# Kernel tuning notes

Hardware: AMD Instinct MI355X
Metric: run time of the kernel (lower is better)

The kernel has to match this reference:

```python
import jax, jax.numpy as jnp
import numpy as np

NUM_CELLS = 16384
NUM_CLASSES = 64
BATCH = 64


def setup_inputs() -> dict:
    key = jax.random.key(0)
    k1, k2 = jax.random.split(key)
    x = jax.random.normal(k1, (BATCH, NUM_CELLS, 1), dtype=jnp.float32)
    weights = jax.random.normal(k2, (NUM_CELLS, NUM_CLASSES, 3), dtype=jnp.float32)
    bias = jnp.zeros((NUM_CELLS, NUM_CLASSES), dtype=jnp.float32)
    return {"x": x, "weights": weights, "bias": bias}


def reference(x, weights, bias):
    # x: (B, N, 1); weights: (N, C, 3); bias: (N, C)
    xs = x[..., 0]                      # (B, N)
    left = jnp.roll(xs, 1, axis=1)      # x[:, i-1]
    right = jnp.roll(xs, -1, axis=1)    # x[:, i+1]
    # out[b,i,c] = left*W[i,c,0] + center*W[i,c,1] + right*W[i,c,2] + bias[i,c]
    out = (left[:, :, None] * weights[:, :, 0]
           + xs[:, :, None] * weights[:, :, 1]
           + right[:, :, None] * weights[:, :, 2]
           + bias)
    return 1.7159 * jnp.tanh(out * (2.0 / 3.0))
```

## Files before the change

kernel.cpp:

```cpp
#include <hip/hip_runtime.h>

#define N_CELLS   16384
#define N_CLASSES 64
#define BATCH     64
#define CPB       4

typedef float f32x4 __attribute__((ext_vector_type(4)));

__device__ __forceinline__ float agm_act(float s) {
    float az = fabsf(s);
    float e  = __expf(-1.3333333333f * az);
    float t  = __fdividef(1.0f - e, 1.0f + e);
    return copysignf(1.7159f * t, s);
}

__global__ __launch_bounds__(256) void mnl_kernel(
    const float* __restrict__ x,
    const float* __restrict__ w,
    const float* __restrict__ bias,
    float* __restrict__ out)
{
    const int t    = threadIdx.x;
    const int lane = t & 63;
    const int wid  = t >> 6;
    const int di   = lane >> 4;
    const int c4   = (lane & 15) * 4;
    const int i    = blockIdx.x * CPB + di;

    const int il = (i == 0)           ? N_CELLS - 1 : i - 1;
    const int ir = (i == N_CELLS - 1) ? 0           : i + 1;

    const float4* wv = reinterpret_cast<const float4*>(
        w + (size_t)i * (N_CLASSES * 3) + (size_t)c4 * 3);
    const float4 v0 = wv[0], v1 = wv[1], v2 = wv[2];
    const float wr[12] = { v0.x, v0.y, v0.z, v0.w,
                           v1.x, v1.y, v1.z, v1.w,
                           v2.x, v2.y, v2.z, v2.w };

    const float4 bi = *reinterpret_cast<const float4*>(
        bias + (size_t)i * N_CLASSES + c4);
    const float bj[4] = { bi.x, bi.y, bi.z, bi.w };

    #pragma unroll 4
    for (int p = 0; p < 16; ++p) {
        const int b = p * 4 + wid;
        const size_t xb = (size_t)b * N_CELLS;

        const float xl = x[xb + il];
        const float xc = x[xb + i];
        const float xr = x[xb + ir];

        f32x4 o;
        o.x = agm_act(fmaf(xl, wr[0], fmaf(xc, wr[1],  fmaf(xr, wr[2],  bj[0]))));
        o.y = agm_act(fmaf(xl, wr[3], fmaf(xc, wr[4],  fmaf(xr, wr[5],  bj[1]))));
        o.z = agm_act(fmaf(xl, wr[6], fmaf(xc, wr[7],  fmaf(xr, wr[8],  bj[2]))));
        o.w = agm_act(fmaf(xl, wr[9], fmaf(xc, wr[10], fmaf(xr, wr[11], bj[3]))));

        f32x4* op = reinterpret_cast<f32x4*>(
            out + ((size_t)b * N_CELLS + i) * N_CLASSES + c4);
        __builtin_nontemporal_store(o, op);
    }
}

extern "C" void kernel_launch(void* const* d_in, const int* in_sizes, int n_in,
                              void* d_out, int out_size, void* d_ws, size_t ws_size,
                              hipStream_t stream) {
    const float* x    = (const float*)d_in[0];
    const float* w    = (const float*)d_in[1];
    const float* bias = (const float*)d_in[2];
    float* out = (float*)d_out;

    dim3 grid(N_CELLS / CPB);
    dim3 block(256);
    mnl_kernel<<<grid, block, 0, stream>>>(x, w, bias, out);
}
```

Baseline: 56.84 us.

## Remap grid to batch-major cell chunks and simplify tanh activation

Each block now handles one batch element and a contiguous chunk of 128 cells, so output writes form one contiguous stream per block. Weights and bias are reloaded per batch element instead of being held in registers and reused across all 64 batches. The activation is rewritten as an exp2 plus hardware reciprocal form of tanh, which removes a division. The trade is much more weight traffic (served from L2 or memory) in exchange for simpler, more contiguous store patterns and a larger grid.

```diff
diff --git a/kernel.cpp b/kernel.cpp
--- a/kernel.cpp
+++ b/kernel.cpp
@@ -3,15 +3,17 @@
 #define N_CELLS   16384
 #define N_CLASSES 64
 #define BATCH     64
-#define CPB       4
+#define CPB       128
 
 typedef float f32x4 __attribute__((ext_vector_type(4)));
+typedef float f32x2 __attribute__((ext_vector_type(2)));
+
+#define K_EXP 1.9235933878f
 
 __device__ __forceinline__ float agm_act(float s) {
-    float az = fabsf(s);
-    float e  = __expf(-1.3333333333f * az);
-    float t  = __fdividef(1.0f - e, 1.0f + e);
-    return copysignf(1.7159f * t, s);
+    float e = __builtin_amdgcn_exp2f(-K_EXP * fabsf(s));
+    float r = __builtin_amdgcn_rcpf(1.0f + e);
+    return copysignf(fmaf(3.4318f, r, -1.7159f), s);
 }
 
 __global__ __launch_bounds__(256) void mnl_kernel(
@@ -20,44 +22,43 @@
     const float* __restrict__ bias,
     float* __restrict__ out)
 {
-    const int t    = threadIdx.x;
-    const int lane = t & 63;
-    const int wid  = t >> 6;
-    const int di   = lane >> 4;
-    const int c4   = (lane & 15) * 4;
-    const int i    = blockIdx.x * CPB + di;
+    const int bid   = blockIdx.x;
+    const int b     = bid >> 7;
+    const int chunk = bid & 127;
+    const int i0    = chunk * CPB;
+    const int t     = threadIdx.x;
 
-    const int il = (i == 0)           ? N_CELLS - 1 : i - 1;
-    const int ir = (i == N_CELLS - 1) ? 0           : i + 1;
-
-    const float4* wv = reinterpret_cast<const float4*>(
-        w + (size_t)i * (N_CLASSES * 3) + (size_t)c4 * 3);
-    const float4 v0 = wv[0], v1 = wv[1], v2 = wv[2];
-    const float wr[12] = { v0.x, v0.y, v0.z, v0.w,
-                           v1.x, v1.y, v1.z, v1.w,
-                           v2.x, v2.y, v2.z, v2.w };
-
-    const float4 bi = *reinterpret_cast<const float4*>(
-        bias + (size_t)i * N_CLASSES + c4);
-    const float bj[4] = { bi.x, bi.y, bi.z, bi.w };
+    const float* __restrict__ xb = x + (size_t)b * N_CELLS;
+    float* __restrict__ ob = out + (size_t)b * N_CELLS * N_CLASSES
+                                 + (size_t)i0 * N_CLASSES;
 
     #pragma unroll 4
-    for (int p = 0; p < 16; ++p) {
-        const int b = p * 4 + wid;
-        const size_t xb = (size_t)b * N_CELLS;
+    for (int it = 0; it < 8; ++it) {
+        const int slot = it * 256 + t;
+        const int cell = slot >> 4;
+        const int quad = slot & 15;
+        const int i    = i0 + cell;
 
-        const float xl = x[xb + il];
-        const float xc = x[xb + i];
-        const float xr = x[xb + ir];
+        const int il = (i == 0)           ? N_CELLS - 1 : i - 1;
+        const int ir = (i == N_CELLS - 1) ? 0           : i + 1;
+
+        const float xl = xb[il];
+        const float xc = xb[i];
+        const float xr = xb[ir];
+
+        const float4* wv = reinterpret_cast<const float4*>(
+            w + (size_t)i * (N_CLASSES * 3) + (size_t)quad * 12);
+        const float4 v0 = wv[0], v1 = wv[1], v2 = wv[2];
+        const float4 bi = *reinterpret_cast<const float4*>(
+            bias + (size_t)i * N_CLASSES + quad * 4);
 
         f32x4 o;
-        o.x = agm_act(fmaf(xl, wr[0], fmaf(xc, wr[1],  fmaf(xr, wr[2],  bj[0]))));
-        o.y = agm_act(fmaf(xl, wr[3], fmaf(xc, wr[4],  fmaf(xr, wr[5],  bj[1]))));
-        o.z = agm_act(fmaf(xl, wr[6], fmaf(xc, wr[7],  fmaf(xr, wr[8],  bj[2]))));
-        o.w = agm_act(fmaf(xl, wr[9], fmaf(xc, wr[10], fmaf(xr, wr[11], bj[3]))));
+        o.x = agm_act(fmaf(xl, v0.x, fmaf(xc, v0.y, fmaf(xr, v0.z, bi.x))));
+        o.y = agm_act(fmaf(xl, v0.w, fmaf(xc, v1.x, fmaf(xr, v1.y, bi.y))));
+        o.z = agm_act(fmaf(xl, v1.z, fmaf(xc, v1.w, fmaf(xr, v2.x, bi.z))));
+        o.w = agm_act(fmaf(xl, v2.y, fmaf(xc, v2.z, fmaf(xr, v2.w, bi.w))));
 
-        f32x4* op = reinterpret_cast<f32x4*>(
-            out + ((size_t)b * N_CELLS + i) * N_CLASSES + c4);
+        f32x4* op = reinterpret_cast<f32x4*>(ob + (size_t)slot * 4);
         __builtin_nontemporal_store(o, op);
     }
 }
@@ -70,7 +71,7 @@
     const float* bias = (const float*)d_in[2];
     float* out = (float*)d_out;
 
-    dim3 grid(N_CELLS / CPB);
+    dim3 grid(BATCH * (N_CELLS / CPB));
     dim3 block(256);
     mnl_kernel<<<grid, block, 0, stream>>>(x, w, bias, out);
 }
```

Result: slower. 63.63 us (+11.9%).
